# Kernel optimization log

Hardware: AMD Instinct MI355X
Metric: run time of the kernel (lower is better)

Reference implementation:

```python
import jax, jax.numpy as jnp
import numpy as np

BATCH = 131072
FEAS = 256
K = 256
DEPTH = 3


def setup_inputs() -> dict:
    key = jax.random.key(0)
    ks = jax.random.split(key, 16)
    # deep tower dims: k//1 -> k//2 -> k//3 -> k//4  == 256 -> 128 -> 85 -> 64
    dims = [K // i for i in range(1, DEPTH + 2)]
    inp = {
        "x": jax.random.normal(ks[0], (BATCH, FEAS), jnp.float32),
        "w_wide": jax.random.normal(ks[1], (FEAS, 1), jnp.float32) * 0.02,
        "b_wide": jnp.zeros((1,), jnp.float32),
        # nn.Parameter(torch.rand(feas, k)) -> uniform [0,1)
        "V": jax.random.uniform(ks[2], (FEAS, K), jnp.float32),
    }
    for i in range(DEPTH):
        fan_in, fan_out = dims[i], dims[i + 1]
        inp[f"w{i+1}"] = jax.random.normal(ks[3 + 2 * i], (fan_in, fan_out), jnp.float32) * (1.0 / np.sqrt(fan_in))
        inp[f"b{i+1}"] = jnp.zeros((fan_out,), jnp.float32)
    inp["w_out"] = jax.random.normal(ks[12], (dims[-1], 1), jnp.float32) * (1.0 / np.sqrt(dims[-1]))
    inp["b_out"] = jnp.zeros((1,), jnp.float32)
    return inp


def reference(x, w_wide, b_wide, V, w1, b1, w2, b2, w3, b3, w_out, b_out):
    # wide (linear) part: [B, 1]
    linear = x @ w_wide + b_wide
    # FM bi-interaction pooling. Original loop: sum_{j >= i} x_i x_j (v_i * v_j)
    # (break/continue on zeros only skip zero-valued terms). Including the
    # diagonal, this equals 0.5 * ((x @ V)^2 + (x^2) @ (V^2)).  [B, K]
    xv = x @ V
    x2v2 = (x * x) @ (V * V)
    tmp = 0.5 * (xv * xv + x2v2)
    # deep tower: Linear + ReLU at each depth
    for w, b in ((w1, b1), (w2, b2), (w3, b3)):
        tmp = jax.nn.relu(tmp @ w + b)
    deep_out = tmp @ w_out + b_out  # [B, 1]
    return jax.nn.sigmoid(linear + deep_out)
```

## Files before the change

kernel.cpp:

```cpp
#include <hip/hip_runtime.h>
#include <math.h>


typedef _Float16 f16;
typedef _Float16 f16x4 __attribute__((ext_vector_type(4)));
typedef _Float16 f16x8 __attribute__((ext_vector_type(8)));
typedef float f32x4 __attribute__((ext_vector_type(4)));

#define NROWS   131072
#define ROWS    64
#define FDIM    256
#define KDIM    256
#define D1      128
#define D2      85
#define D2P     96

#define OFF_VT_H   0x0UL
#define OFF_VT_L   0x20000UL
#define OFF_V2T    0x40000UL
#define OFF_W1T_H  0x60000UL
#define OFF_W1T_L  0x70000UL
#define OFF_W2T_H  0x80000UL
#define OFF_W2T_L  0x86000UL
#define OFF_W3T_H  0x8C000UL
#define OFF_W3T_L  0x8F000UL

static __device__ __forceinline__ f32x4 mfma16(f16x8 a, f16x8 b, f32x4 c) {
  return __builtin_amdgcn_mfma_f32_16x16x32_f16(a, b, c, 0, 0, 0);
}

__global__ __launch_bounds__(256) void prep_kernel(
    const float* __restrict__ V, const float* __restrict__ w1,
    const float* __restrict__ w2, const float* __restrict__ w3,
    f16* VT_h, f16* VT_l, f16* V2T,
    f16* W1T_h, f16* W1T_l, f16* W2T_h, f16* W2T_l, f16* W3T_h, f16* W3T_l) {
  int idx0 = blockIdx.x * 256 + threadIdx.x;
  int stride = gridDim.x * 256;
  for (int idx = idx0; idx < KDIM * FDIM; idx += stride) {
    int i = idx >> 8, k = idx & 255;
    float v = V[idx];
    f16 h = (f16)v;
    int o = k * FDIM + i;
    VT_h[o] = h;
    VT_l[o] = (f16)(v - (float)h);
    V2T[o] = (f16)(v * v);
  }
  for (int idx = idx0; idx < D1 * KDIM; idx += stride) {
    int k = idx >> 7, n = idx & 127;
    float w = w1[idx];
    f16 h = (f16)w;
    int o = n * KDIM + k;
    W1T_h[o] = h;
    W1T_l[o] = (f16)(w - (float)h);
  }
  for (int idx = idx0; idx < D2P * D1; idx += stride) {
    int n = idx >> 7, k = idx & 127;
    float w = (n < D2) ? w2[k * D2 + n] : 0.f;
    f16 h = (f16)w;
    W2T_h[idx] = h;
    W2T_l[idx] = (f16)(w - (float)h);
  }
  for (int idx = idx0; idx < 64 * D2P; idx += stride) {
    int n = idx / D2P, k = idx - n * D2P;
    float w = (k < D2) ? w3[k * 64 + n] : 0.f;
    f16 h = (f16)w;
    W3T_h[idx] = h;
    W3T_l[idx] = (f16)(w - (float)h);
  }
}

__global__ __launch_bounds__(512, 4) void fused_kernel(
    const float* __restrict__ x, const float* __restrict__ w_wide,
    const float* __restrict__ b_wide,
    const f16* __restrict__ VT_h, const f16* __restrict__ VT_l,
    const f16* __restrict__ V2T,
    const f16* __restrict__ W1T_h, const f16* __restrict__ W1T_l,
    const float* __restrict__ b1,
    const f16* __restrict__ W2T_h, const f16* __restrict__ W2T_l,
    const float* __restrict__ b2,
    const f16* __restrict__ W3T_h, const f16* __restrict__ W3T_l,
    const float* __restrict__ b3,
    const float* __restrict__ w_out, const float* __restrict__ b_out,
    float* __restrict__ out) {
  __shared__ __align__(16) f16 smem[32768];
  __shared__ float linS[ROWS];
  __shared__ float pfS[ROWS * 2];

  f16* sXh  = smem;
  f16* sXl  = smem + 8192;
  f16* sX2  = smem + 16384;
  f16* tmpH = smem;
  f16* tmpL = smem + 16384;
  f16* h1H  = smem + 16384;
  f16* h1L  = smem + 24576;
  f16* h2H  = smem;
  f16* h2L  = smem + 8192;

  const int tid = threadIdx.x;
  const int lane = tid & 63, wv = tid >> 6;
  const int q = lane >> 4, ln = lane & 15;
  const int row0 = blockIdx.x * ROWS;
  const int sr = tid >> 3, sc = (tid & 7) * 16;

  f32x4 accV[4][2], acc2[4][2];
#pragma unroll
  for (int i = 0; i < 4; ++i)
#pragma unroll
    for (int j = 0; j < 2; ++j) {
      accV[i][j] = (f32x4){0.f, 0.f, 0.f, 0.f};
      acc2[i][j] = (f32x4){0.f, 0.f, 0.f, 0.f};
    }
  float linp = 0.f;

  for (int kk = 0; kk < 2; ++kk) {
    const int kbase = kk * 128;
    float4 a[4], w4[4];
    const float* xp = x + (size_t)(row0 + sr) * FDIM + kbase + sc;
    const float* wp = w_wide + kbase + sc;
#pragma unroll
    for (int t = 0; t < 4; ++t) {
      a[t] = *(const float4*)(xp + t * 4);
      w4[t] = *(const float4*)(wp + t * 4);
    }
    __syncthreads();
#pragma unroll
    for (int t = 0; t < 4; ++t) {
      linp += a[t].x * w4[t].x + a[t].y * w4[t].y + a[t].z * w4[t].z +
              a[t].w * w4[t].w;
      float f0[4] = {a[t].x, a[t].y, a[t].z, a[t].w};
      f16x4 h0, l0, q0;
#pragma unroll
      for (int j = 0; j < 4; ++j) {
        f16 h = (f16)f0[j];
        h0[j] = h;
        l0[j] = (f16)(f0[j] - (float)h);
        q0[j] = (f16)(f0[j] * f0[j]);
      }
      int u = (sc + t * 4) >> 3;
      int usw = u ^ (sr & 15);
      int off0 = sr * 128 + (usw << 3) + ((t & 1) << 2);
      *(f16x4*)(sXh + off0) = h0;
      *(f16x4*)(sXl + off0) = l0;
      *(f16x4*)(sX2 + off0) = q0;
    }
    __syncthreads();

#pragma unroll
    for (int ks = 0; ks < 4; ++ks) {
      const int k0 = kbase + ks * 32;
      f16x8 Bh[2], Bl[2], B2[2];
#pragma unroll
      for (int ni = 0; ni < 2; ++ni) {
        int n = wv * 32 + ni * 16 + ln;
        size_t boff = (size_t)n * FDIM + k0 + q * 8;
        Bh[ni] = *(const f16x8*)(VT_h + boff);
        Bl[ni] = *(const f16x8*)(VT_l + boff);
        B2[ni] = *(const f16x8*)(V2T + boff);
      }
#pragma unroll
      for (int mi = 0; mi < 4; ++mi) {
        int aoff = (mi * 16 + ln) * 128 + ((((ks << 2) + q) ^ ln) << 3);
        f16x8 Ah = *(const f16x8*)(sXh + aoff);
        f16x8 Al = *(const f16x8*)(sXl + aoff);
        f16x8 A2 = *(const f16x8*)(sX2 + aoff);
#pragma unroll
        for (int ni = 0; ni < 2; ++ni) {
          accV[mi][ni] = mfma16(Al, Bh[ni], accV[mi][ni]);
          accV[mi][ni] = mfma16(Ah, Bl[ni], accV[mi][ni]);
          accV[mi][ni] = mfma16(Ah, Bh[ni], accV[mi][ni]);
          acc2[mi][ni] = mfma16(A2, B2[ni], acc2[mi][ni]);
        }
      }
    }
  }

  {
    float s0 = linp;
    s0 += __shfl_xor(s0, 1);
    s0 += __shfl_xor(s0, 2);
    s0 += __shfl_xor(s0, 4);
    if ((tid & 7) == 0) linS[sr] = s0 + b_wide[0];
  }

  __syncthreads();

#pragma unroll
  for (int mi = 0; mi < 4; ++mi)
#pragma unroll
    for (int r = 0; r < 4; ++r) {
      int m = mi * 16 + q * 4 + r;
      int mrow = m * 256, msw = m & 7;
#pragma unroll
      for (int ni = 0; ni < 2; ++ni) {
        int n = wv * 32 + ni * 16 + ln;
        float xv = accV[mi][ni][r];
        float val = 0.5f * (xv * xv + acc2[mi][ni][r]);
        f16 hi = (f16)val;
        f16 lo = (f16)(val - (float)hi);
        int off = mrow + (((n >> 3) ^ msw) << 3) + (n & 7);
        tmpH[off] = hi;
        tmpL[off] = lo;
      }
    }

  __syncthreads();

  f32x4 acc1[4];
#pragma unroll
  for (int i = 0; i < 4; ++i) acc1[i] = (f32x4){0.f, 0.f, 0.f, 0.f};

#pragma unroll
  for (int ks = 0; ks < 8; ++ks) {
    size_t boff = (size_t)(wv * 16 + ln) * KDIM + ks * 32 + q * 8;
    f16x8 Bh = *(const f16x8*)(W1T_h + boff);
    f16x8 Bl = *(const f16x8*)(W1T_l + boff);
#pragma unroll
    for (int mi = 0; mi < 4; ++mi) {
      int m = mi * 16 + ln;
      int aoff = m * 256 + (((ks * 4 + q) ^ (m & 7)) << 3);
      f16x8 Ah = *(const f16x8*)(tmpH + aoff);
      f16x8 Al = *(const f16x8*)(tmpL + aoff);
      acc1[mi] = mfma16(Al, Bh, acc1[mi]);
      acc1[mi] = mfma16(Ah, Bl, acc1[mi]);
      acc1[mi] = mfma16(Ah, Bh, acc1[mi]);
    }
  }

  __syncthreads();

  {
    int n = wv * 16 + ln;
    float bias = b1[n];
#pragma unroll
    for (int mi = 0; mi < 4; ++mi)
#pragma unroll
      for (int r = 0; r < 4; ++r) {
        int m = mi * 16 + q * 4 + r;
        float z = acc1[mi][r] + bias;
        z = z > 0.f ? z : 0.f;
        f16 hi = (f16)z;
        f16 lo = (f16)(z - (float)hi);
        int off = m * 128 + (((n >> 3) ^ (m & 7)) << 3) + (n & 7);
        h1H[off] = hi;
        h1L[off] = lo;
      }
  }

  __syncthreads();

  const int mt = wv & 3, half = wv >> 2;
  f32x4 accL2[3];
#pragma unroll
  for (int j = 0; j < 3; ++j) accL2[j] = (f32x4){0.f, 0.f, 0.f, 0.f};

#pragma unroll
  for (int ks = 0; ks < 4; ++ks) {
    int m = mt * 16 + ln;
    int aoff = m * 128 + (((ks * 4 + q) ^ (m & 7)) << 3);
    f16x8 Ah = *(const f16x8*)(h1H + aoff);
    f16x8 Al = *(const f16x8*)(h1L + aoff);
#pragma unroll
    for (int nj = 0; nj < 3; ++nj) {
      int n = (half * 3 + nj) * 16 + ln;
      size_t boff = (size_t)n * D1 + ks * 32 + q * 8;
      f16x8 Bh = *(const f16x8*)(W2T_h + boff);
      f16x8 Bl = *(const f16x8*)(W2T_l + boff);
      accL2[nj] = mfma16(Al, Bh, accL2[nj]);
      accL2[nj] = mfma16(Ah, Bl, accL2[nj]);
      accL2[nj] = mfma16(Ah, Bh, accL2[nj]);
    }
  }

#pragma unroll
  for (int r = 0; r < 4; ++r) {
    int m = mt * 16 + q * 4 + r;
    int mrow = m * 128, msw = m & 7;
#pragma unroll
    for (int nj = 0; nj < 3; ++nj) {
      int n = (half * 3 + nj) * 16 + ln;
      float z = accL2[nj][r] + ((n < D2) ? b2[n] : 0.f);
      z = z > 0.f ? z : 0.f;
      f16 hi = (f16)z;
      f16 lo = (f16)(z - (float)hi);
      int off = mrow + (((n >> 3) ^ msw) << 3) + (n & 7);
      h2H[off] = hi;
      h2L[off] = lo;
    }
  }

  __syncthreads();

  f32x4 accL3[2];
  accL3[0] = (f32x4){0.f, 0.f, 0.f, 0.f};
  accL3[1] = (f32x4){0.f, 0.f, 0.f, 0.f};

#pragma unroll
  for (int ks = 0; ks < 3; ++ks) {
    int m = mt * 16 + ln;
    int aoff = m * 128 + (((ks * 4 + q) ^ (m & 7)) << 3);
    f16x8 Ah = *(const f16x8*)(h2H + aoff);
    f16x8 Al = *(const f16x8*)(h2L + aoff);
#pragma unroll
    for (int nj = 0; nj < 2; ++nj) {
      int n = (half * 2 + nj) * 16 + ln;
      size_t boff = (size_t)n * D2P + ks * 32 + q * 8;
      f16x8 Bh = *(const f16x8*)(W3T_h + boff);
      f16x8 Bl = *(const f16x8*)(W3T_l + boff);
      accL3[nj] = mfma16(Al, Bh, accL3[nj]);
      accL3[nj] = mfma16(Ah, Bl, accL3[nj]);
      accL3[nj] = mfma16(Ah, Bh, accL3[nj]);
    }
  }

  {
    float b3v[2], wov[2];
#pragma unroll
    for (int nj = 0; nj < 2; ++nj) {
      int n = (half * 2 + nj) * 16 + ln;
      b3v[nj] = b3[n];
      wov[nj] = w_out[n];
    }
#pragma unroll
    for (int r = 0; r < 4; ++r) {
      float part = 0.f;
#pragma unroll
      for (int nj = 0; nj < 2; ++nj) {
        float z = accL3[nj][r] + b3v[nj];
        part += (z > 0.f ? z : 0.f) * wov[nj];
      }
      part += __shfl_xor(part, 1);
      part += __shfl_xor(part, 2);
      part += __shfl_xor(part, 4);
      part += __shfl_xor(part, 8);
      if (ln == 0) pfS[(mt * 16 + q * 4 + r) * 2 + half] = part;
    }
  }

  __syncthreads();

  if (tid < ROWS) {
    float zf = linS[tid] + pfS[tid * 2] + pfS[tid * 2 + 1] + b_out[0];
    out[row0 + tid] = 1.f / (1.f + expf(-zf));
  }
}

extern "C" void kernel_launch(void* const* d_in, const int* in_sizes, int n_in,
                              void* d_out, int out_size, void* d_ws, size_t ws_size,
                              hipStream_t stream) {
  const float* x = (const float*)d_in[0];
  const float* w_wide = (const float*)d_in[1];
  const float* b_wide = (const float*)d_in[2];
  const float* V = (const float*)d_in[3];
  const float* w1 = (const float*)d_in[4];
  const float* b1 = (const float*)d_in[5];
  const float* w2 = (const float*)d_in[6];
  const float* b2 = (const float*)d_in[7];
  const float* w3 = (const float*)d_in[8];
  const float* b3 = (const float*)d_in[9];
  const float* w_out = (const float*)d_in[10];
  const float* b_out = (const float*)d_in[11];
  float* out = (float*)d_out;
  char* ws = (char*)d_ws;

  f16* VT_h = (f16*)(ws + OFF_VT_H);
  f16* VT_l = (f16*)(ws + OFF_VT_L);
  f16* V2T = (f16*)(ws + OFF_V2T);
  f16* W1T_h = (f16*)(ws + OFF_W1T_H);
  f16* W1T_l = (f16*)(ws + OFF_W1T_L);
  f16* W2T_h = (f16*)(ws + OFF_W2T_H);
  f16* W2T_l = (f16*)(ws + OFF_W2T_L);
  f16* W3T_h = (f16*)(ws + OFF_W3T_H);
  f16* W3T_l = (f16*)(ws + OFF_W3T_L);

  prep_kernel<<<256, 256, 0, stream>>>(V, w1, w2, w3, VT_h, VT_l, V2T, W1T_h,
                                       W1T_l, W2T_h, W2T_l, W3T_h, W3T_l);

  fused_kernel<<<NROWS / ROWS, 512, 0, stream>>>(
      x, w_wide, b_wide, VT_h, VT_l, V2T, W1T_h, W1T_l, b1, W2T_h, W2T_l, b2,
      W3T_h, W3T_l, b3, w_out, b_out, out);
}
```

Before: 380.4 us.

## Double-buffer x staging in 64-wide chunks and change LDS swizzle for tower layers

Splits the x load and f16 hi/lo/square conversion into four 64-column chunks held in two ping-ponged LDS buffers. Global loads for the next chunk are issued while the current chunk's MFMAs run, overlapping memory latency with compute and dropping one barrier. The tower-layer LDS swizzle also changes to a new XOR pattern (FSW) meant to cut bank conflicts on the hi/lo activation writes and reads. The cost is more register pressure from the prefetched float4s and more complex indexing, which could reduce occupancy at launch bound 512x4.

```diff
diff --git a/kernel.cpp b/kernel.cpp
--- a/kernel.cpp
+++ b/kernel.cpp
@@ -3,7 +3,6 @@
 
 
 typedef _Float16 f16;
-typedef _Float16 f16x4 __attribute__((ext_vector_type(4)));
 typedef _Float16 f16x8 __attribute__((ext_vector_type(8)));
 typedef float f32x4 __attribute__((ext_vector_type(4)));
 
@@ -14,6 +13,8 @@
 #define D1      128
 #define D2      85
 #define D2P     96
+
+#define FSW(mm) ((((mm) & 7)) ^ ((((mm) >> 3) & 1) << 1))
 
 #define OFF_VT_H   0x0UL
 #define OFF_VT_L   0x20000UL
@@ -86,9 +87,6 @@
   __shared__ float linS[ROWS];
   __shared__ float pfS[ROWS * 2];
 
-  f16* sXh  = smem;
-  f16* sXl  = smem + 8192;
-  f16* sX2  = smem + 16384;
   f16* tmpH = smem;
   f16* tmpL = smem + 16384;
   f16* h1H  = smem + 16384;
@@ -100,7 +98,10 @@
   const int lane = tid & 63, wv = tid >> 6;
   const int q = lane >> 4, ln = lane & 15;
   const int row0 = blockIdx.x * ROWS;
-  const int sr = tid >> 3, sc = (tid & 7) * 16;
+  const int srow = tid >> 3;
+  const int u8 = (tid & 7) << 3;
+  const int stg = srow * 64 + (((tid & 7) ^ (srow & 7)) << 3);
+  const int fr = (ln & 7) ^ (((ln >> 3) & 1) << 1);
 
   f32x4 accV[4][2], acc2[4][2];
 #pragma unroll
@@ -112,42 +113,51 @@
     }
   float linp = 0.f;
 
-  for (int kk = 0; kk < 2; ++kk) {
-    const int kbase = kk * 128;
-    float4 a[4], w4[4];
-    const float* xp = x + (size_t)(row0 + sr) * FDIM + kbase + sc;
-    const float* wp = w_wide + kbase + sc;
-#pragma unroll
-    for (int t = 0; t < 4; ++t) {
-      a[t] = *(const float4*)(xp + t * 4);
-      w4[t] = *(const float4*)(wp + t * 4);
-    }
-    __syncthreads();
-#pragma unroll
-    for (int t = 0; t < 4; ++t) {
-      linp += a[t].x * w4[t].x + a[t].y * w4[t].y + a[t].z * w4[t].z +
-              a[t].w * w4[t].w;
-      float f0[4] = {a[t].x, a[t].y, a[t].z, a[t].w};
-      f16x4 h0, l0, q0;
-#pragma unroll
-      for (int j = 0; j < 4; ++j) {
-        f16 h = (f16)f0[j];
-        h0[j] = h;
-        l0[j] = (f16)(f0[j] - (float)h);
-        q0[j] = (f16)(f0[j] * f0[j]);
-      }
-      int u = (sc + t * 4) >> 3;
-      int usw = u ^ (sr & 15);
-      int off0 = sr * 128 + (usw << 3) + ((t & 1) << 2);
-      *(f16x4*)(sXh + off0) = h0;
-      *(f16x4*)(sXl + off0) = l0;
-      *(f16x4*)(sX2 + off0) = q0;
-    }
-    __syncthreads();
-
-#pragma unroll
-    for (int ks = 0; ks < 4; ++ks) {
-      const int k0 = kbase + ks * 32;
+  float4 aP[2][2], wP[2][2];
+
+#define LOADG(C, P)                                                         \
+  {                                                                         \
+    const float* xp = x + (size_t)(row0 + srow) * FDIM + (C) * 64 + u8;     \
+    const float* wp = w_wide + (C) * 64 + u8;                               \
+    aP[P][0] = *(const float4*)(xp);                                        \
+    aP[P][1] = *(const float4*)(xp + 4);                                    \
+    wP[P][0] = *(const float4*)(wp);                                        \
+    wP[P][1] = *(const float4*)(wp + 4);                                    \
+  }
+
+#define STAGE(P)                                                            \
+  {                                                                         \
+    f16* bb = smem + (P) * 12288;                                           \
+    float v[8] = {aP[P][0].x, aP[P][0].y, aP[P][0].z, aP[P][0].w,           \
+                  aP[P][1].x, aP[P][1].y, aP[P][1].z, aP[P][1].w};          \
+    float w[8] = {wP[P][0].x, wP[P][0].y, wP[P][0].z, wP[P][0].w,           \
+                  wP[P][1].x, wP[P][1].y, wP[P][1].z, wP[P][1].w};          \
+    f16x8 hh, ll, ss;                                                       \
+    _Pragma("unroll") for (int j = 0; j < 8; ++j) {                         \
+      linp += v[j] * w[j];                                                  \
+      f16 h = (f16)v[j];                                                    \
+      hh[j] = h;                                                            \
+      ll[j] = (f16)(v[j] - (float)h);                                       \
+      ss[j] = (f16)(v[j] * v[j]);                                           \
+    }                                                                       \
+    *(f16x8*)(bb + stg) = hh;                                               \
+    *(f16x8*)(bb + 4096 + stg) = ll;                                        \
+    *(f16x8*)(bb + 8192 + stg) = ss;                                        \
+  }
+
+  LOADG(0, 0);
+  STAGE(0);
+  LOADG(1, 1);
+  __syncthreads();
+
+#pragma unroll
+  for (int c = 0; c < 4; ++c) {
+    if (c < 2) LOADG(c + 2, c & 1);
+    if (c < 3) STAGE((c + 1) & 1);
+    f16* sb = smem + (c & 1) * 12288;
+#pragma unroll
+    for (int ksl = 0; ksl < 2; ++ksl) {
+      const int k0 = c * 64 + ksl * 32;
       f16x8 Bh[2], Bl[2], B2[2];
 #pragma unroll
       for (int ni = 0; ni < 2; ++ni) {
@@ -159,10 +169,10 @@
       }
 #pragma unroll
       for (int mi = 0; mi < 4; ++mi) {
-        int aoff = (mi * 16 + ln) * 128 + ((((ks << 2) + q) ^ ln) << 3);
-        f16x8 Ah = *(const f16x8*)(sXh + aoff);
-        f16x8 Al = *(const f16x8*)(sXl + aoff);
-        f16x8 A2 = *(const f16x8*)(sX2 + aoff);
+        int aoff = (mi * 16 + ln) * 64 + ((((ksl << 2) + q) ^ (ln & 7)) << 3);
+        f16x8 Ah = *(const f16x8*)(sb + aoff);
+        f16x8 Al = *(const f16x8*)(sb + 4096 + aoff);
+        f16x8 A2 = *(const f16x8*)(sb + 8192 + aoff);
 #pragma unroll
         for (int ni = 0; ni < 2; ++ni) {
           accV[mi][ni] = mfma16(Al, Bh[ni], accV[mi][ni]);
@@ -172,24 +182,25 @@
         }
       }
     }
-  }
+    __syncthreads();
+  }
+#undef LOADG
+#undef STAGE
 
   {
     float s0 = linp;
     s0 += __shfl_xor(s0, 1);
     s0 += __shfl_xor(s0, 2);
     s0 += __shfl_xor(s0, 4);
-    if ((tid & 7) == 0) linS[sr] = s0 + b_wide[0];
-  }
-
-  __syncthreads();
+    if ((tid & 7) == 0) linS[srow] = s0 + b_wide[0];
+  }
 
 #pragma unroll
   for (int mi = 0; mi < 4; ++mi)
 #pragma unroll
     for (int r = 0; r < 4; ++r) {
       int m = mi * 16 + q * 4 + r;
-      int mrow = m * 256, msw = m & 7;
+      int mrow = m * 256, fw = FSW(q * 4 + r);
 #pragma unroll
       for (int ni = 0; ni < 2; ++ni) {
         int n = wv * 32 + ni * 16 + ln;
@@ -197,7 +208,7 @@
         float val = 0.5f * (xv * xv + acc2[mi][ni][r]);
         f16 hi = (f16)val;
         f16 lo = (f16)(val - (float)hi);
-        int off = mrow + (((n >> 3) ^ msw) << 3) + (n & 7);
+        int off = mrow + (((n >> 3) ^ fw) << 3) + (n & 7);
         tmpH[off] = hi;
         tmpL[off] = lo;
       }
@@ -217,7 +228,7 @@
 #pragma unroll
     for (int mi = 0; mi < 4; ++mi) {
       int m = mi * 16 + ln;
-      int aoff = m * 256 + (((ks * 4 + q) ^ (m & 7)) << 3);
+      int aoff = m * 256 + (((ks * 4 + q) ^ fr) << 3);
       f16x8 Ah = *(const f16x8*)(tmpH + aoff);
       f16x8 Al = *(const f16x8*)(tmpL + aoff);
       acc1[mi] = mfma16(Al, Bh, acc1[mi]);
@@ -240,7 +251,7 @@
         z = z > 0.f ? z : 0.f;
         f16 hi = (f16)z;
         f16 lo = (f16)(z - (float)hi);
-        int off = m * 128 + (((n >> 3) ^ (m & 7)) << 3) + (n & 7);
+        int off = m * 128 + (((n >> 3) ^ FSW(q * 4 + r)) << 3) + (n & 7);
         h1H[off] = hi;
         h1L[off] = lo;
       }
@@ -256,7 +267,7 @@
 #pragma unroll
   for (int ks = 0; ks < 4; ++ks) {
     int m = mt * 16 + ln;
-    int aoff = m * 128 + (((ks * 4 + q) ^ (m & 7)) << 3);
+    int aoff = m * 128 + (((ks * 4 + q) ^ fr) << 3);
     f16x8 Ah = *(const f16x8*)(h1H + aoff);
     f16x8 Al = *(const f16x8*)(h1L + aoff);
 #pragma unroll
@@ -274,7 +285,7 @@
 #pragma unroll
   for (int r = 0; r < 4; ++r) {
     int m = mt * 16 + q * 4 + r;
-    int mrow = m * 128, msw = m & 7;
+    int mrow = m * 128, fw = FSW(q * 4 + r);
 #pragma unroll
     for (int nj = 0; nj < 3; ++nj) {
       int n = (half * 3 + nj) * 16 + ln;
@@ -282,7 +293,7 @@
       z = z > 0.f ? z : 0.f;
       f16 hi = (f16)z;
       f16 lo = (f16)(z - (float)hi);
-      int off = mrow + (((n >> 3) ^ msw) << 3) + (n & 7);
+      int off = mrow + (((n >> 3) ^ fw) << 3) + (n & 7);
       h2H[off] = hi;
       h2L[off] = lo;
     }
@@ -297,7 +308,7 @@
 #pragma unroll
   for (int ks = 0; ks < 3; ++ks) {
     int m = mt * 16 + ln;
-    int aoff = m * 128 + (((ks * 4 + q) ^ (m & 7)) << 3);
+    int aoff = m * 128 + (((ks * 4 + q) ^ fr) << 3);
     f16x8 Ah = *(const f16x8*)(h2H + aoff);
     f16x8 Al = *(const f16x8*)(h2L + aoff);
 #pragma unroll
```

Result: no change. 379.8 us (-0.1%).
